# Kernel tuning notes

Measured on AMD Instinct MI355X. Metric: run time of the kernel, lower is better.

Reference implementation:

```python
import jax, jax.numpy as jnp
import numpy as np

B, CIN, N, E = 8192, 16, 96, 768
NF, EMB, NCLS = 64, 128, 210


def _p(key, shape, scale=0.05):
    return jax.random.normal(key, shape, dtype=jnp.float32) * scale


def setup_inputs() -> dict:
    key = jax.random.key(0)
    ks = jax.random.split(key, 20)
    return {
        "src": jax.random.normal(ks[0], (B, CIN, N), dtype=jnp.float32),
        "edge_index": jax.random.randint(ks[1], (2, E), 0, N, dtype=jnp.int32),
        "gcn1_w": _p(ks[2], (CIN, 64)), "gcn1_b": _p(ks[3], (64,)),
        "gcn2_w": _p(ks[4], (64, 32)), "gcn2_b": _p(ks[5], (32,)),
        "conv1_w": _p(ks[6], (NF, 32, 7)), "conv1_b": _p(ks[7], (NF,)),
        "conv2_w": _p(ks[8], (NF * 2, NF, 5)), "conv2_b": _p(ks[9], (NF * 2,)),
        "conv3_w": _p(ks[10], (NF * 4, NF * 2, 3)), "conv3_b": _p(ks[11], (NF * 4,)),
        "fc1_w": _p(ks[12], (3072, EMB)), "fc1_b": _p(ks[13], (EMB,)),
        "cls1_w": _p(ks[14], (EMB, EMB)), "cls1_b": _p(ks[15], (EMB,)),
        "cls2_w": _p(ks[16], (EMB, NCLS)), "cls2_b": _p(ks[17], (NCLS,)),
    }


def gcn_conv(x, edge_index, W, b):
    n = x.shape[1]
    loops = jnp.arange(n, dtype=edge_index.dtype)
    row = jnp.concatenate([edge_index[0], loops])  # targets
    col = jnp.concatenate([edge_index[1], loops])  # sources
    deg = jnp.zeros((n,), x.dtype).at[row].add(1.0)
    dinv = jax.lax.rsqrt(jnp.maximum(deg, 1e-12))
    norm = dinv[row] * dinv[col]                 # [E+N]
    h = x @ W                                    # [B, N, Fout]
    msgs = h[:, col, :] * norm[None, :, None]    # gather along node dim
    out = jnp.zeros_like(h).at[:, row, :].add(msgs)  # scatter-add
    return out + b


def conv1d(x, w, b, stride, pad):
    # x: [B, C, L], w: [O, C, K]
    y = jax.lax.conv_general_dilated(x, w, (stride,), [(pad, pad)],
                                     dimension_numbers=("NCH", "OIH", "NCH"))
    return y + b[None, :, None]


def reference(src, edge_index, gcn1_w, gcn1_b, gcn2_w, gcn2_b,
              conv1_w, conv1_b, conv2_w, conv2_b, conv3_w, conv3_b,
              fc1_w, fc1_b, cls1_w, cls1_b, cls2_w, cls2_b):
    x = jnp.transpose(src, (0, 2, 1))            # [B, N, CIN]
    x = jax.nn.relu(gcn_conv(x, edge_index, gcn1_w, gcn1_b))
    x = jax.nn.relu(gcn_conv(x, edge_index, gcn2_w, gcn2_b))
    x = jnp.transpose(x, (0, 2, 1))              # [B, 32, N]
    x = jax.nn.relu(conv1d(x, conv1_w, conv1_b, 2, 3))
    x = jax.nn.relu(conv1d(x, conv2_w, conv2_b, 2, 2))
    x = jax.nn.relu(conv1d(x, conv3_w, conv3_b, 2, 1))
    x = x.reshape(x.shape[0], -1)                # [B, 3072]
    feat = x @ fc1_w + fc1_b
    x = jax.nn.relu(feat)
    x = jax.nn.relu(x @ cls1_w + cls1_b)
    x = x @ cls2_w + cls2_b
    return (x, feat)
```

## Files before the change

kernel.cpp:

```cpp
#include <hip/hip_runtime.h>


typedef __attribute__((ext_vector_type(8))) short short8v;
typedef __attribute__((ext_vector_type(4))) float floatx4;

#define N_NODE 96
#define E_TOT  864
#define BATCH  8192ull

#define R0_OFF   0ull
#define R1_OFF   25165824ull
#define FR_OFF   50331648ull
#define R2_OFF   51380224ull
#define WT_OFF   52428800ull
#define W1N_OFF  (WT_OFF + 0)
#define W2N_OFF  (WT_OFF + 2048)
#define WC1_OFF  (WT_OFF + 4096)
#define WC2_OFF  (WT_OFF + 18432)
#define WC3_OFF  (WT_OFF + 59392)
#define WF1_OFF  (WT_OFF + 157696)
#define WL1_OFF  (WT_OFF + 550912)
#define WL2_OFF  (WT_OFF + 567296)
#define AH_OFF   (WT_OFF + 600064)

__device__ __forceinline__ unsigned short f2b(float f) {
    unsigned int u = __builtin_bit_cast(unsigned int, f);
    u += 0x7fffu + ((u >> 16) & 1u);
    return (unsigned short)(u >> 16);
}
__device__ __forceinline__ float b2f(unsigned short h) {
    unsigned int u = ((unsigned int)h) << 16;
    return __builtin_bit_cast(float, u);
}

__global__ void prep_all(const int* __restrict__ eidx,
                         const float* __restrict__ g1w, const float* __restrict__ g2w,
                         const float* __restrict__ w1, const float* __restrict__ w2,
                         const float* __restrict__ w3, const float* __restrict__ f1,
                         const float* __restrict__ l1, const float* __restrict__ l2,
                         unsigned short* __restrict__ wt,
                         unsigned short* __restrict__ ahf) {
    const int tid = threadIdx.x;
    if (blockIdx.x < 36) {
        __shared__ int   rowv[E_TOT];
        __shared__ int   colv[E_TOT];
        __shared__ int   rcv[E_TOT];
        __shared__ float val[E_TOT];
        __shared__ float dinv[N_NODE];
        for (int e = tid; e < E_TOT; e += 256) {
            int r, c;
            if (e < 768) { r = eidx[e]; c = eidx[768 + e]; }
            else         { r = e - 768; c = r; }
            rowv[e] = r; colv[e] = c; rcv[e] = r * 96 + c;
        }
        __syncthreads();
        if (tid < N_NODE) {
            int d = 0;
            for (int e = 0; e < E_TOT; e++) d += (rowv[e] == tid) ? 1 : 0;
            dinv[tid] = rsqrtf(fmaxf((float)d, 1e-12f));
        }
        __syncthreads();
        for (int e = tid; e < E_TOT; e += 256)
            val[e] = dinv[rowv[e]] * dinv[colv[e]];
        __syncthreads();
        int i = blockIdx.x * 256 + tid;
        int f = i >> 9, rm = i & 511;
        int ln = rm >> 3, j = rm & 7;
        int fm = f / 3, kk = f % 3;
        int row = fm * 16 + (ln & 15);
        int col = kk * 32 + (ln >> 4) * 8 + j;
        int cell = row * 96 + col;
        float a = 0.f;
        for (int e = 0; e < E_TOT; e++)
            a += (rcv[e] == cell) ? val[e] : 0.f;
        unsigned short hi = f2b(a);
        ahf[i] = hi;
        ahf[9216 + i] = f2b(a - b2f(hi));
        return;
    }
    long idx = (long)(blockIdx.x - 36) * 256 + tid;
    if (idx >= 600064) return;
    float v;
    if (idx < 2048) {
        int o = idx >> 5, c = idx & 31;
        v = (c < 16) ? g1w[c * 64 + o] : 0.f;
    } else if (idx < 4096) {
        long j = idx - 2048; int g = j >> 6, c = j & 63;
        v = g2w[c * 32 + g];
    } else {
        long base, KS;
        int region;
        if      (idx < 18432)  { base = 4096;   KS = 7;  region = 0; }
        else if (idx < 59392)  { base = 18432;  KS = 10; region = 1; }
        else if (idx < 157696) { base = 59392;  KS = 12; region = 2; }
        else if (idx < 550912) { base = 157696; KS = 96; region = 3; }
        else if (idx < 567296) { base = 550912; KS = 4;  region = 4; }
        else                   { base = 567296; KS = 4;  region = 5; }
        long local = idx - base;
        long g  = local / (KS * 512);
        long rm = local % (KS * 512);
        long ks = rm / 512;
        int lane = (int)((rm % 512) / 8);
        int j    = (int)(rm % 8);
        int quad = lane >> 4, n16 = lane & 15;
        int n = (int)(g * 16 + n16);
        int k = (int)(ks * 32 + quad * 8 + j);
        switch (region) {
            case 0: { int t = k / 32,  c = k % 32;  v = w1[n * 224 + c * 7 + t]; } break;
            case 1: { int t = k / 64,  c = k % 64;  v = w2[n * 320 + c * 5 + t]; } break;
            case 2: { int t = k / 128, c = k % 128; v = w3[n * 384 + c * 3 + t]; } break;
            case 3: { int t = k / 256, o = k % 256; v = f1[(o * 12 + t) * 128 + n]; } break;
            case 4: v = l1[k * 128 + n]; break;
            default: v = (n < 210) ? l2[k * 210 + n] : 0.f; break;
        }
    }
    wt[idx] = f2b(v);
}

__launch_bounds__(256, 4)
__global__ void gcn_fused(const float* __restrict__ src,
                          const unsigned short* __restrict__ ahf,
                          const unsigned short* __restrict__ w1n,
                          const unsigned short* __restrict__ w2n,
                          const float* __restrict__ b1,
                          const float* __restrict__ b2,
                          unsigned short* __restrict__ h2) {
    __shared__ __align__(16) unsigned short pool[4 * 4864];
    const int tid = threadIdx.x;
    const int w = tid >> 6, lane = tid & 63, quad = lane >> 4, m16 = lane & 15;
    unsigned short* P   = pool + w * 4864;
    unsigned short* XAc = P;
    unsigned short* H1W = P + 384;
    unsigned short* HWT = P + 1536;
    unsigned short* Cw  = P;
    const size_t bb = (size_t)blockIdx.x * 4 + w;

    *(unsigned int*)&XAc[(lane >> 2) * 24 + 16 + (lane & 3) * 2] = 0;

    short8v w1f[4], w2f[2][2];
    float bv1[4], bv2[2];
#pragma unroll
    for (int fn = 0; fn < 4; fn++) {
        w1f[fn] = *(const short8v*)&w1n[(fn * 16 + m16) * 32 + quad * 8];
        bv1[fn] = b1[fn * 16 + m16];
    }
#pragma unroll
    for (int fn = 0; fn < 2; fn++) {
#pragma unroll
        for (int kk = 0; kk < 2; kk++)
            w2f[fn][kk] = *(const short8v*)&w2n[(fn * 16 + m16) * 64 + kk * 32 + quad * 8];
        bv2[fn] = b2[fn * 16 + m16];
    }

    floatx4 acc[6] = {};
    const float* sB = src + bb * 1536 + (size_t)m16 * 96;
#pragma unroll
    for (int kk = 0; kk < 3; kk++) {
        float4 f0 = *(const float4*)&sB[kk * 32 + quad * 8];
        float4 f1 = *(const float4*)&sB[kk * 32 + quad * 8 + 4];
        float fv[8] = {f0.x, f0.y, f0.z, f0.w, f1.x, f1.y, f1.z, f1.w};
        short8v bh, bl;
#pragma unroll
        for (int j = 0; j < 8; j++) {
            unsigned short hi = f2b(fv[j]);
            bh[j] = (short)hi;
            bl[j] = (short)f2b(fv[j] - b2f(hi));
        }
#pragma unroll
        for (int fm = 0; fm < 6; fm++) {
            short8v ah = *(const short8v*)&ahf[((fm * 3 + kk) << 9) + lane * 8];
            short8v al = *(const short8v*)&ahf[9216 + ((fm * 3 + kk) << 9) + lane * 8];
            acc[fm] = __builtin_amdgcn_mfma_f32_16x16x32_bf16(ah, bh, acc[fm], 0, 0, 0);
            acc[fm] = __builtin_amdgcn_mfma_f32_16x16x32_bf16(al, bh, acc[fm], 0, 0, 0);
            acc[fm] = __builtin_amdgcn_mfma_f32_16x16x32_bf16(ah, bl, acc[fm], 0, 0, 0);
        }
    }

#pragma unroll
    for (int cc = 0; cc < 6; cc++) {
#pragma unroll
        for (int r = 0; r < 4; r++)
            XAc[(quad * 4 + r) * 24 + m16] = f2b(acc[cc][r]);
        short8v afr1 = *(const short8v*)&XAc[m16 * 24 + quad * 8];
        floatx4 a1[4];
#pragma unroll
        for (int fn = 0; fn < 4; fn++) {
            floatx4 zc = {0.f, 0.f, 0.f, 0.f};
            a1[fn] = __builtin_amdgcn_mfma_f32_16x16x32_bf16(afr1, w1f[fn], zc, 0, 0, 0);
        }
#pragma unroll
        for (int fn = 0; fn < 4; fn++)
#pragma unroll
            for (int r = 0; r < 4; r++)
                H1W[(quad * 4 + r) * 72 + fn * 16 + m16] =
                    f2b(fmaxf(a1[fn][r] + bv1[fn], 0.f));
        floatx4 a2[2] = {};
#pragma unroll
        for (int kk = 0; kk < 2; kk++) {
            short8v afr2 = *(const short8v*)&H1W[m16 * 72 + kk * 32 + quad * 8];
#pragma unroll
            for (int fn = 0; fn < 2; fn++)
                a2[fn] = __builtin_amdgcn_mfma_f32_16x16x32_bf16(afr2, w2f[fn][kk], a2[fn], 0, 0, 0);
        }
#pragma unroll
        for (int fn = 0; fn < 2; fn++)
#pragma unroll
            for (int r = 0; r < 4; r++)
                HWT[(fn * 16 + m16) * 104 + cc * 16 + quad * 4 + r] = f2b(a2[fn][r]);
    }

    floatx4 c2a[6][2] = {};
#pragma unroll
    for (int kk = 0; kk < 3; kk++) {
        short8v bfr[2];
#pragma unroll
        for (int fn = 0; fn < 2; fn++)
            bfr[fn] = *(const short8v*)&HWT[(fn * 16 + m16) * 104 + kk * 32 + quad * 8];
#pragma unroll
        for (int fm = 0; fm < 6; fm++) {
            short8v ah = *(const short8v*)&ahf[((fm * 3 + kk) << 9) + lane * 8];
            short8v al = *(const short8v*)&ahf[9216 + ((fm * 3 + kk) << 9) + lane * 8];
#pragma unroll
            for (int fn = 0; fn < 2; fn++) {
                c2a[fm][fn] = __builtin_amdgcn_mfma_f32_16x16x32_bf16(ah, bfr[fn], c2a[fm][fn], 0, 0, 0);
                c2a[fm][fn] = __builtin_amdgcn_mfma_f32_16x16x32_bf16(al, bfr[fn], c2a[fm][fn], 0, 0, 0);
            }
        }
    }
#pragma unroll
    for (int fm = 0; fm < 6; fm++)
#pragma unroll
        for (int fn = 0; fn < 2; fn++)
#pragma unroll
            for (int r = 0; r < 4; r++)
                Cw[(fm * 16 + quad * 4 + r) * 32 + fn * 16 + m16] =
                    f2b(fmaxf(c2a[fm][fn][r] + bv2[fn], 0.f));
#pragma unroll
    for (int it = 0; it < 6; it++) {
        int idx = it * 64 + lane;
        int node = idx >> 2, q8 = idx & 3;
        *(uint4*)&h2[((size_t)node * BATCH + bb) * 32 + q8 * 8] =
            *(const uint4*)&Cw[idx * 8];
    }
}

template<int WM, int FN, int NTAP, int CIN, int NOUT, int STRIDE, int PAD, int LIN, int BK, int MODE>
__launch_bounds__(256)
__global__ void gemm_slab(const unsigned short* __restrict__ in,
                          const unsigned short* __restrict__ wn,
                          const float* __restrict__ bias,
                          unsigned short* __restrict__ outb,
                          float* __restrict__ outf) {
    constexpr int BM  = WM * 32;
    constexpr int BN  = FN * 32;
    constexpr int BKP = BK + 8;
    constexpr int CPT = CIN / BK;
    constexpr int NC  = NTAP * CPT;
    constexpr int KS  = NTAP * CIN / 32;
    constexpr int NV  = BM * BK / 8 / 256;
    constexpr int RPV = 256 / (BK / 8);
    constexpr int SZ1 = 2 * BM * BKP;
    constexpr int SZ2 = (MODE == 4) ? 16 : BM * (BN + 8);
    constexpr int POOL = SZ1 > SZ2 ? SZ1 : SZ2;
    __shared__ __align__(16) unsigned short pool[POOL];
    const int tid = threadIdx.x;
    const size_t b0 = blockIdx.x * BM;
    const int n0 = blockIdx.y * BN;
    const int l  = blockIdx.z;
    const int w = tid >> 6, lane = tid & 63, quad = lane >> 4, m16 = lane & 15;
    const int wm = w >> 1, wq = w & 1;
    const int mbase = wm * (WM * 16), nbase = wq * (FN * 16);
    const int gw = (n0 + nbase) >> 4;
    const int lr = tid / (BK / 8);
    const int lc = tid % (BK / 8);
    floatx4 acc[WM][FN] = {};
    const short8v zz8 = {0, 0, 0, 0, 0, 0, 0, 0};

    short8v pre[NV], nxt[NV];
    {
        int pos = STRIDE * l - PAD;
        if (pos >= 0 && pos < LIN) {
            const unsigned short* ag = in + ((size_t)pos * BATCH + b0) * CIN;
#pragma unroll
            for (int v = 0; v < NV; v++)
                pre[v] = *(const short8v*)&ag[(size_t)(lr + v * RPV) * CIN + lc * 8];
        } else {
#pragma unroll
            for (int v = 0; v < NV; v++) pre[v] = zz8;
        }
#pragma unroll
        for (int v = 0; v < NV; v++)
            *(short8v*)&pool[(lr + v * RPV) * BKP + lc * 8] = pre[v];
    }
    int p = 0;
#pragma unroll
    for (int ch = 0; ch < NC; ++ch) {
        __syncthreads();
        if (ch + 1 < NC) {
            int t = (ch + 1) / CPT, inner = (ch + 1) % CPT;
            int pos = STRIDE * l + t - PAD;
            if (pos >= 0 && pos < LIN) {
                const unsigned short* ag = in + ((size_t)pos * BATCH + b0) * CIN + inner * BK;
#pragma unroll
                for (int v = 0; v < NV; v++)
                    nxt[v] = *(const short8v*)&ag[(size_t)(lr + v * RPV) * CIN + lc * 8];
            } else {
#pragma unroll
                for (int v = 0; v < NV; v++) nxt[v] = zz8;
            }
        }
        const unsigned short* As = pool + p * BM * BKP;
        const int kbase = (ch / CPT) * CIN + (ch % CPT) * BK;
#pragma unroll
        for (int kk = 0; kk < BK; kk += 32) {
            const int ksG = (kbase + kk) >> 5;
            short8v bfr[FN];
#pragma unroll
            for (int fn = 0; fn < FN; fn++)
                bfr[fn] = *(const short8v*)&wn[(((size_t)(gw + fn) * KS + ksG) << 9) + lane * 8];
#pragma unroll
            for (int fm = 0; fm < WM; fm++) {
                short8v afr = *(const short8v*)&As[(mbase + fm * 16 + m16) * BKP + kk + quad * 8];
#pragma unroll
                for (int fn = 0; fn < FN; fn++)
                    acc[fm][fn] = __builtin_amdgcn_mfma_f32_16x16x32_bf16(afr, bfr[fn], acc[fm][fn], 0, 0, 0);
            }
        }
        if (ch + 1 < NC) {
            unsigned short* Ad = pool + (p ^ 1) * BM * BKP;
#pragma unroll
            for (int v = 0; v < NV; v++)
                *(short8v*)&Ad[(lr + v * RPV) * BKP + lc * 8] = nxt[v];
        }
        p ^= 1;
    }

    if constexpr (MODE == 4) {
#pragma unroll
        for (int fn = 0; fn < FN; fn++) {
            int cg = n0 + nbase + fn * 16 + m16;
            float bv = (cg < 210) ? bias[cg] : 0.f;
            if (cg < 210) {
#pragma unroll
                for (int fm = 0; fm < WM; fm++)
#pragma unroll
                    for (int r = 0; r < 4; r++) {
                        size_t row = b0 + mbase + fm * 16 + quad * 4 + r;
                        outf[row * 210 + cg] = acc[fm][fn][r] + bv;
                    }
            }
        }
    } else {
        float bv[FN];
#pragma unroll
        for (int fn = 0; fn < FN; fn++) bv[fn] = bias[n0 + nbase + fn * 16 + m16];
        __syncthreads();
        unsigned short* Cs = pool;
#pragma unroll
        for (int fm = 0; fm < WM; fm++)
#pragma unroll
            for (int r = 0; r < 4; r++) {
                int row = mbase + fm * 16 + quad * 4 + r;
#pragma unroll
                for (int fn = 0; fn < FN; fn++)
                    Cs[row * (BN + 8) + nbase + fn * 16 + m16] =
                        f2b(fmaxf(acc[fm][fn][r] + bv[fn], 0.f));
            }
        __syncthreads();
        for (int u = tid; u < BM * (BN / 8); u += 256) {
            int r = u / (BN / 8), cc = u % (BN / 8);
            *(short8v*)&outb[((size_t)l * BATCH + b0 + r) * NOUT + n0 + cc * 8] =
                *(short8v*)&Cs[r * (BN + 8) + cc * 8];
        }
    }
}

__launch_bounds__(256)
__global__ void fc1_splitk(const unsigned short* __restrict__ c3,
                           const unsigned short* __restrict__ wf1,
                           float* __restrict__ part) {
    __shared__ __align__(16) unsigned short pool[2 * 128 * 72];
    const int tid = threadIdx.x;
    const size_t b0 = blockIdx.x * 128;
    const int kg = blockIdx.z;
    const int w = tid >> 6, lane = tid & 63, quad = lane >> 4, m16 = lane & 15;
    const int wm = w >> 1, wq = w & 1;
    const int mbase = wm * 64, nbase = wq * 64;
    const int gw = nbase >> 4;
    const int lr = tid >> 3, lc = tid & 7;
    floatx4 acc[4][4] = {};
    short8v pre[4], nxt[4];

    {
        const unsigned short* ag = c3 + ((size_t)(kg * 2) * BATCH + b0) * 256;
#pragma unroll
        for (int v = 0; v < 4; v++)
            pre[v] = *(const short8v*)&ag[(size_t)(lr + v * 32) * 256 + lc * 8];
#pragma unroll
        for (int v = 0; v < 4; v++)
            *(short8v*)&pool[(lr + v * 32) * 72 + lc * 8] = pre[v];
    }
    int p = 0;
#pragma unroll
    for (int s = 0; s < 8; ++s) {
        __syncthreads();
        if (s + 1 < 8) {
            int t = kg * 2 + ((s + 1) >> 2), inner = (s + 1) & 3;
            const unsigned short* ag = c3 + ((size_t)t * BATCH + b0) * 256 + inner * 64;
#pragma unroll
            for (int v = 0; v < 4; v++)
                nxt[v] = *(const short8v*)&ag[(size_t)(lr + v * 32) * 256 + lc * 8];
        }
        const unsigned short* As = pool + p * 128 * 72;
        const int kbase = (kg * 2 + (s >> 2)) * 256 + (s & 3) * 64;
#pragma unroll
        for (int kk = 0; kk < 64; kk += 32) {
            const int ksG = (kbase + kk) >> 5;
            short8v bfr[4];
#pragma unroll
            for (int fn = 0; fn < 4; fn++)
                bfr[fn] = *(const short8v*)&wf1[(((size_t)(gw + fn) * 96 + ksG) << 9) + lane * 8];
#pragma unroll
            for (int fm = 0; fm < 4; fm++) {
                short8v afr = *(const short8v*)&As[(mbase + fm * 16 + m16) * 72 + kk + quad * 8];
#pragma unroll
                for (int fn = 0; fn < 4; fn++)
                    acc[fm][fn] = __builtin_amdgcn_mfma_f32_16x16x32_bf16(afr, bfr[fn], acc[fm][fn], 0, 0, 0);
            }
        }
        if (s + 1 < 8) {
            unsigned short* Ad = pool + (p ^ 1) * 128 * 72;
#pragma unroll
            for (int v = 0; v < 4; v++)
                *(short8v*)&Ad[(lr + v * 32) * 72 + lc * 8] = nxt[v];
        }
        p ^= 1;
    }
    float* pg = part + (size_t)kg * BATCH * 128;
#pragma unroll
    for (int fm = 0; fm < 4; fm++)
#pragma unroll
        for (int r = 0; r < 4; r++) {
            size_t row = b0 + mbase + fm * 16 + quad * 4 + r;
#pragma unroll
            for (int fn = 0; fn < 4; fn++)
                pg[row * 128 + nbase + fn * 16 + m16] = acc[fm][fn][r];
        }
}

__launch_bounds__(256)
__global__ void fc1_reduce(const float* __restrict__ part, const float* __restrict__ bias,
                           float* __restrict__ feat, unsigned short* __restrict__ fr) {
    const size_t idx = (size_t)blockIdx.x * 256 + threadIdx.x;
    const size_t row = idx >> 5;
    const int    c4  = (int)(idx & 31);
    float4 s = *(const float4*)&bias[c4 * 4];
#pragma unroll
    for (int z = 0; z < 6; z++) {
        float4 p = *(const float4*)&part[(z * BATCH + row) * 128 + c4 * 4];
        s.x += p.x; s.y += p.y; s.z += p.z; s.w += p.w;
    }
    *(float4*)&feat[row * 128 + c4 * 4] = s;
    unsigned int d0 = (unsigned int)f2b(fmaxf(s.x, 0.f)) |
                      ((unsigned int)f2b(fmaxf(s.y, 0.f)) << 16);
    unsigned int d1 = (unsigned int)f2b(fmaxf(s.z, 0.f)) |
                      ((unsigned int)f2b(fmaxf(s.w, 0.f)) << 16);
    *(uint2*)&fr[row * 128 + c4 * 4] = make_uint2(d0, d1);
}

extern "C" void kernel_launch(void* const* d_in, const int* in_sizes, int n_in,
                              void* d_out, int out_size, void* d_ws, size_t ws_size,
                              hipStream_t stream) {
    const float* src  = (const float*)d_in[0];
    const int*   eidx = (const int*)  d_in[1];
    const float* g1w  = (const float*)d_in[2];
    const float* g1b  = (const float*)d_in[3];
    const float* g2w  = (const float*)d_in[4];
    const float* g2b  = (const float*)d_in[5];
    const float* cv1w = (const float*)d_in[6];
    const float* cv1b = (const float*)d_in[7];
    const float* cv2w = (const float*)d_in[8];
    const float* cv2b = (const float*)d_in[9];
    const float* cv3w = (const float*)d_in[10];
    const float* cv3b = (const float*)d_in[11];
    const float* fc1w = (const float*)d_in[12];
    const float* fc1b = (const float*)d_in[13];
    const float* cl1w = (const float*)d_in[14];
    const float* cl1b = (const float*)d_in[15];
    const float* cl2w = (const float*)d_in[16];
    const float* cl2b = (const float*)d_in[17];

    unsigned short* ws16 = (unsigned short*)d_ws;
    float* wsF = (float*)d_ws;
    float* out = (float*)d_out;

    unsigned short* h2  = ws16 + R0_OFF;
    unsigned short* c1  = ws16 + R1_OFF;
    unsigned short* c2  = ws16 + R0_OFF;
    unsigned short* c3  = ws16 + R1_OFF;
    float*          part = wsF;
    unsigned short* fr  = ws16 + FR_OFF;
    unsigned short* r2  = ws16 + R2_OFF;
    unsigned short* w1n = ws16 + W1N_OFF;
    unsigned short* w2n = ws16 + W2N_OFF;
    unsigned short* wc1 = ws16 + WC1_OFF;
    unsigned short* wc2 = ws16 + WC2_OFF;
    unsigned short* wc3 = ws16 + WC3_OFF;
    unsigned short* wf1 = ws16 + WF1_OFF;
    unsigned short* wl1 = ws16 + WL1_OFF;
    unsigned short* wl2 = ws16 + WL2_OFF;
    unsigned short* ahf = ws16 + AH_OFF;

    float* feat_out = out + 8192ull * 210ull;

    prep_all<<<2380, 256, 0, stream>>>(eidx, g1w, g2w, cv1w, cv2w, cv3w, fc1w, cl1w, cl2w,
                                       ws16 + WT_OFF, ahf);
    gcn_fused<<<2048, 256, 0, stream>>>(src, ahf, w1n, w2n, g1b, g2b, h2);
    gemm_slab<8, 2, 7, 32, 64, 2, 3, 96, 32, 0>
        <<<dim3(32, 1, 48), 256, 0, stream>>>(h2, wc1, cv1b, c1, nullptr);
    gemm_slab<4, 4, 5, 64, 128, 2, 2, 48, 64, 0>
        <<<dim3(64, 1, 24), 256, 0, stream>>>(c1, wc2, cv2b, c2, nullptr);
    gemm_slab<4, 4, 3, 128, 256, 2, 1, 24, 64, 0>
        <<<dim3(64, 2, 12), 256, 0, stream>>>(c2, wc3, cv3b, c3, nullptr);
    fc1_splitk<<<dim3(64, 1, 6), 256, 0, stream>>>(c3, wf1, part);
    fc1_reduce<<<1024, 256, 0, stream>>>(part, fc1b, feat_out, fr);
    gemm_slab<2, 2, 1, 128, 128, 1, 0, 1, 64, 0>
        <<<dim3(128, 2, 1), 256, 0, stream>>>(fr, wl1, cl1b, r2, nullptr);
    gemm_slab<2, 2, 1, 128, 256, 1, 0, 1, 64, 4>
        <<<dim3(128, 4, 1), 256, 0, stream>>>(r2, wl2, cl2b, nullptr, out);
}
```

Measured before the change: 334.8 us.

## Fuse fc1 reduce with classifier GEMMs and process two samples per GCN wave

Replaces the fc1 split-K reduce kernel and the two small classifier GEMM launches with one cls_fused kernel. It sums the partials, writes feat, and runs both classifier layers from shared memory, so the fr and r2 intermediates no longer go through global memory and two launches are removed. Separately, gcn_fused now handles two batch samples per wavefront, which reuses the adjacency fragment loads across both samples and halves the grid. The cost is doubled LDS per block and more registers (launch bounds lowered to 2 blocks), which lowers occupancy.

```diff
diff --git a/kernel.cpp b/kernel.cpp
--- a/kernel.cpp
+++ b/kernel.cpp
@@ -117,7 +117,7 @@
     wt[idx] = f2b(v);
 }
 
-__launch_bounds__(256, 4)
+__launch_bounds__(256, 2)
 __global__ void gcn_fused(const float* __restrict__ src,
                           const unsigned short* __restrict__ ahf,
                           const unsigned short* __restrict__ w1n,
@@ -125,17 +125,15 @@
                           const float* __restrict__ b1,
                           const float* __restrict__ b2,
                           unsigned short* __restrict__ h2) {
-    __shared__ __align__(16) unsigned short pool[4 * 4864];
+    __shared__ __align__(16) unsigned short pool[4 * 9728];
     const int tid = threadIdx.x;
     const int w = tid >> 6, lane = tid & 63, quad = lane >> 4, m16 = lane & 15;
-    unsigned short* P   = pool + w * 4864;
-    unsigned short* XAc = P;
-    unsigned short* H1W = P + 384;
-    unsigned short* HWT = P + 1536;
-    unsigned short* Cw  = P;
-    const size_t bb = (size_t)blockIdx.x * 4 + w;
-
-    *(unsigned int*)&XAc[(lane >> 2) * 24 + 16 + (lane & 3) * 2] = 0;
+    unsigned short* P = pool + w * 9728;
+    const size_t bb0 = (size_t)blockIdx.x * 8 + w * 2;
+
+#pragma unroll
+    for (int b = 0; b < 2; b++)
+        *(unsigned int*)&P[b * 4864 + (lane >> 2) * 24 + 16 + (lane & 3) * 2] = 0;
 
     short8v w1f[4], w2f[2][2];
     float bv1[4], bv2[2];
@@ -152,95 +150,133 @@
         bv2[fn] = b2[fn * 16 + m16];
     }
 
-    floatx4 acc[6] = {};
-    const float* sB = src + bb * 1536 + (size_t)m16 * 96;
+    floatx4 acc[2][6] = {};
 #pragma unroll
     for (int kk = 0; kk < 3; kk++) {
-        float4 f0 = *(const float4*)&sB[kk * 32 + quad * 8];
-        float4 f1 = *(const float4*)&sB[kk * 32 + quad * 8 + 4];
-        float fv[8] = {f0.x, f0.y, f0.z, f0.w, f1.x, f1.y, f1.z, f1.w};
-        short8v bh, bl;
-#pragma unroll
-        for (int j = 0; j < 8; j++) {
-            unsigned short hi = f2b(fv[j]);
-            bh[j] = (short)hi;
-            bl[j] = (short)f2b(fv[j] - b2f(hi));
+        short8v bh[2], bl[2];
+#pragma unroll
+        for (int b = 0; b < 2; b++) {
+            const float* sB = src + (bb0 + b) * 1536 + (size_t)m16 * 96;
+            float4 f0 = *(const float4*)&sB[kk * 32 + quad * 8];
+            float4 f1 = *(const float4*)&sB[kk * 32 + quad * 8 + 4];
+            float fv[8] = {f0.x, f0.y, f0.z, f0.w, f1.x, f1.y, f1.z, f1.w};
+#pragma unroll
+            for (int j = 0; j < 8; j++) {
+                unsigned short hi = f2b(fv[j]);
+                bh[b][j] = (short)hi;
+                bl[b][j] = (short)f2b(fv[j] - b2f(hi));
+            }
         }
 #pragma unroll
         for (int fm = 0; fm < 6; fm++) {
             short8v ah = *(const short8v*)&ahf[((fm * 3 + kk) << 9) + lane * 8];
             short8v al = *(const short8v*)&ahf[9216 + ((fm * 3 + kk) << 9) + lane * 8];
-            acc[fm] = __builtin_amdgcn_mfma_f32_16x16x32_bf16(ah, bh, acc[fm], 0, 0, 0);
-            acc[fm] = __builtin_amdgcn_mfma_f32_16x16x32_bf16(al, bh, acc[fm], 0, 0, 0);
-            acc[fm] = __builtin_amdgcn_mfma_f32_16x16x32_bf16(ah, bl, acc[fm], 0, 0, 0);
+#pragma unroll
+            for (int b = 0; b < 2; b++) {
+                acc[b][fm] = __builtin_amdgcn_mfma_f32_16x16x32_bf16(ah, bh[b], acc[b][fm], 0, 0, 0);
+                acc[b][fm] = __builtin_amdgcn_mfma_f32_16x16x32_bf16(al, bh[b], acc[b][fm], 0, 0, 0);
+                acc[b][fm] = __builtin_amdgcn_mfma_f32_16x16x32_bf16(ah, bl[b], acc[b][fm], 0, 0, 0);
+            }
         }
     }
 
 #pragma unroll
     for (int cc = 0; cc < 6; cc++) {
-#pragma unroll
-        for (int r = 0; r < 4; r++)
-            XAc[(quad * 4 + r) * 24 + m16] = f2b(acc[cc][r]);
-        short8v afr1 = *(const short8v*)&XAc[m16 * 24 + quad * 8];
-        floatx4 a1[4];
-#pragma unroll
-        for (int fn = 0; fn < 4; fn++) {
-            floatx4 zc = {0.f, 0.f, 0.f, 0.f};
-            a1[fn] = __builtin_amdgcn_mfma_f32_16x16x32_bf16(afr1, w1f[fn], zc, 0, 0, 0);
-        }
-#pragma unroll
-        for (int fn = 0; fn < 4; fn++)
+        short8v afr1[2];
+#pragma unroll
+        for (int b = 0; b < 2; b++) {
+            unsigned short* XAc = P + b * 4864;
 #pragma unroll
             for (int r = 0; r < 4; r++)
-                H1W[(quad * 4 + r) * 72 + fn * 16 + m16] =
-                    f2b(fmaxf(a1[fn][r] + bv1[fn], 0.f));
-        floatx4 a2[2] = {};
-#pragma unroll
-        for (int kk = 0; kk < 2; kk++) {
-            short8v afr2 = *(const short8v*)&H1W[m16 * 72 + kk * 32 + quad * 8];
+                XAc[(quad * 4 + r) * 24 + m16] = f2b(acc[b][cc][r]);
+            afr1[b] = *(const short8v*)&XAc[m16 * 24 + quad * 8];
+        }
+        floatx4 a1[2][4];
+#pragma unroll
+        for (int b = 0; b < 2; b++)
+#pragma unroll
+            for (int fn = 0; fn < 4; fn++) {
+                floatx4 zc = {0.f, 0.f, 0.f, 0.f};
+                a1[b][fn] = __builtin_amdgcn_mfma_f32_16x16x32_bf16(afr1[b], w1f[fn], zc, 0, 0, 0);
+            }
+#pragma unroll
+        for (int b = 0; b < 2; b++) {
+            unsigned short* H1W = P + b * 4864 + 384;
+#pragma unroll
+            for (int fn = 0; fn < 4; fn++)
+#pragma unroll
+                for (int r = 0; r < 4; r++)
+                    H1W[(quad * 4 + r) * 72 + fn * 16 + m16] =
+                        f2b(fmaxf(a1[b][fn][r] + bv1[fn], 0.f));
+        }
+        floatx4 a2[2][2] = {};
+#pragma unroll
+        for (int kk = 0; kk < 2; kk++)
+#pragma unroll
+            for (int b = 0; b < 2; b++) {
+                const unsigned short* H1W = P + b * 4864 + 384;
+                short8v afr2 = *(const short8v*)&H1W[m16 * 72 + kk * 32 + quad * 8];
+#pragma unroll
+                for (int fn = 0; fn < 2; fn++)
+                    a2[b][fn] = __builtin_amdgcn_mfma_f32_16x16x32_bf16(afr2, w2f[fn][kk], a2[b][fn], 0, 0, 0);
+            }
+#pragma unroll
+        for (int b = 0; b < 2; b++) {
+            unsigned short* HWT = P + b * 4864 + 1536;
 #pragma unroll
             for (int fn = 0; fn < 2; fn++)
-                a2[fn] = __builtin_amdgcn_mfma_f32_16x16x32_bf16(afr2, w2f[fn][kk], a2[fn], 0, 0, 0);
-        }
-#pragma unroll
-        for (int fn = 0; fn < 2; fn++)
-#pragma unroll
-            for (int r = 0; r < 4; r++)
-                HWT[(fn * 16 + m16) * 104 + cc * 16 + quad * 4 + r] = f2b(a2[fn][r]);
-    }
-
-    floatx4 c2a[6][2] = {};
+#pragma unroll
+                for (int r = 0; r < 4; r++)
+                    HWT[(fn * 16 + m16) * 104 + cc * 16 + quad * 4 + r] = f2b(a2[b][fn][r]);
+        }
+    }
+
+    floatx4 c2a[2][6][2] = {};
 #pragma unroll
     for (int kk = 0; kk < 3; kk++) {
-        short8v bfr[2];
-#pragma unroll
-        for (int fn = 0; fn < 2; fn++)
-            bfr[fn] = *(const short8v*)&HWT[(fn * 16 + m16) * 104 + kk * 32 + quad * 8];
+        short8v bfr[2][2];
+#pragma unroll
+        for (int b = 0; b < 2; b++) {
+            const unsigned short* HWT = P + b * 4864 + 1536;
+#pragma unroll
+            for (int fn = 0; fn < 2; fn++)
+                bfr[b][fn] = *(const short8v*)&HWT[(fn * 16 + m16) * 104 + kk * 32 + quad * 8];
+        }
 #pragma unroll
         for (int fm = 0; fm < 6; fm++) {
             short8v ah = *(const short8v*)&ahf[((fm * 3 + kk) << 9) + lane * 8];
             short8v al = *(const short8v*)&ahf[9216 + ((fm * 3 + kk) << 9) + lane * 8];
 #pragma unroll
-            for (int fn = 0; fn < 2; fn++) {
-                c2a[fm][fn] = __builtin_amdgcn_mfma_f32_16x16x32_bf16(ah, bfr[fn], c2a[fm][fn], 0, 0, 0);
-                c2a[fm][fn] = __builtin_amdgcn_mfma_f32_16x16x32_bf16(al, bfr[fn], c2a[fm][fn], 0, 0, 0);
-            }
-        }
-    }
-#pragma unroll
-    for (int fm = 0; fm < 6; fm++)
-#pragma unroll
-        for (int fn = 0; fn < 2; fn++)
-#pragma unroll
-            for (int r = 0; r < 4; r++)
-                Cw[(fm * 16 + quad * 4 + r) * 32 + fn * 16 + m16] =
-                    f2b(fmaxf(c2a[fm][fn][r] + bv2[fn], 0.f));
-#pragma unroll
-    for (int it = 0; it < 6; it++) {
-        int idx = it * 64 + lane;
-        int node = idx >> 2, q8 = idx & 3;
-        *(uint4*)&h2[((size_t)node * BATCH + bb) * 32 + q8 * 8] =
-            *(const uint4*)&Cw[idx * 8];
+            for (int b = 0; b < 2; b++)
+#pragma unroll
+                for (int fn = 0; fn < 2; fn++) {
+                    c2a[b][fm][fn] = __builtin_amdgcn_mfma_f32_16x16x32_bf16(ah, bfr[b][fn], c2a[b][fm][fn], 0, 0, 0);
+                    c2a[b][fm][fn] = __builtin_amdgcn_mfma_f32_16x16x32_bf16(al, bfr[b][fn], c2a[b][fm][fn], 0, 0, 0);
+                }
+        }
+    }
+#pragma unroll
+    for (int b = 0; b < 2; b++) {
+        unsigned short* Cw = P + b * 4864;
+#pragma unroll
+        for (int fm = 0; fm < 6; fm++)
+#pragma unroll
+            for (int fn = 0; fn < 2; fn++)
+#pragma unroll
+                for (int r = 0; r < 4; r++)
+                    Cw[(fm * 16 + quad * 4 + r) * 32 + fn * 16 + m16] =
+                        f2b(fmaxf(c2a[b][fm][fn][r] + bv2[fn], 0.f));
+    }
+#pragma unroll
+    for (int b = 0; b < 2; b++) {
+        const unsigned short* Cw = P + b * 4864;
+#pragma unroll
+        for (int it = 0; it < 6; it++) {
+            int idx = it * 64 + lane;
+            int node = idx >> 2, q8 = idx & 3;
+            *(uint4*)&h2[((size_t)node * BATCH + bb0 + b) * 32 + q8 * 8] =
+                *(const uint4*)&Cw[idx * 8];
+        }
     }
 }
 
@@ -449,23 +485,95 @@
 }
 
 __launch_bounds__(256)
-__global__ void fc1_reduce(const float* __restrict__ part, const float* __restrict__ bias,
-                           float* __restrict__ feat, unsigned short* __restrict__ fr) {
-    const size_t idx = (size_t)blockIdx.x * 256 + threadIdx.x;
-    const size_t row = idx >> 5;
-    const int    c4  = (int)(idx & 31);
-    float4 s = *(const float4*)&bias[c4 * 4];
-#pragma unroll
-    for (int z = 0; z < 6; z++) {
-        float4 p = *(const float4*)&part[(z * BATCH + row) * 128 + c4 * 4];
-        s.x += p.x; s.y += p.y; s.z += p.z; s.w += p.w;
-    }
-    *(float4*)&feat[row * 128 + c4 * 4] = s;
-    unsigned int d0 = (unsigned int)f2b(fmaxf(s.x, 0.f)) |
-                      ((unsigned int)f2b(fmaxf(s.y, 0.f)) << 16);
-    unsigned int d1 = (unsigned int)f2b(fmaxf(s.z, 0.f)) |
-                      ((unsigned int)f2b(fmaxf(s.w, 0.f)) << 16);
-    *(uint2*)&fr[row * 128 + c4 * 4] = make_uint2(d0, d1);
+__global__ void cls_fused(const float* __restrict__ part, const float* __restrict__ fbias,
+                          const unsigned short* __restrict__ wl1, const float* __restrict__ bl1,
+                          const unsigned short* __restrict__ wl2, const float* __restrict__ bl2,
+                          float* __restrict__ feat, float* __restrict__ outp) {
+    __shared__ __align__(16) unsigned short frL[32 * 136];
+    __shared__ __align__(16) unsigned short r2L[32 * 136];
+    const int tid = threadIdx.x;
+    const size_t b0 = (size_t)blockIdx.x * 32;
+    const int w = tid >> 6, lane = tid & 63, quad = lane >> 4, m16 = lane & 15;
+
+#pragma unroll
+    for (int u = tid; u < 1024; u += 256) {
+        int row = u >> 5, c4 = u & 31;
+        float4 s = *(const float4*)&fbias[c4 * 4];
+#pragma unroll
+        for (int z = 0; z < 6; z++) {
+            float4 p = *(const float4*)&part[((size_t)z * BATCH + b0 + row) * 128 + c4 * 4];
+            s.x += p.x; s.y += p.y; s.z += p.z; s.w += p.w;
+        }
+        *(float4*)&feat[(b0 + row) * 128 + c4 * 4] = s;
+        unsigned int d0 = (unsigned int)f2b(fmaxf(s.x, 0.f)) |
+                          ((unsigned int)f2b(fmaxf(s.y, 0.f)) << 16);
+        unsigned int d1 = (unsigned int)f2b(fmaxf(s.z, 0.f)) |
+                          ((unsigned int)f2b(fmaxf(s.w, 0.f)) << 16);
+        *(unsigned int*)&frL[row * 136 + c4 * 4]     = d0;
+        *(unsigned int*)&frL[row * 136 + c4 * 4 + 2] = d1;
+    }
+    __syncthreads();
+
+    {
+        const int nbase = w * 32;
+        floatx4 acc[2][2] = {};
+#pragma unroll
+        for (int ks = 0; ks < 4; ks++) {
+            short8v bfr[2];
+#pragma unroll
+            for (int fn = 0; fn < 2; fn++)
+                bfr[fn] = *(const short8v*)&wl1[(((size_t)(w * 2 + fn) * 4 + ks) << 9) + lane * 8];
+#pragma unroll
+            for (int fm = 0; fm < 2; fm++) {
+                short8v afr = *(const short8v*)&frL[(fm * 16 + m16) * 136 + ks * 32 + quad * 8];
+#pragma unroll
+                for (int fn = 0; fn < 2; fn++)
+                    acc[fm][fn] = __builtin_amdgcn_mfma_f32_16x16x32_bf16(afr, bfr[fn], acc[fm][fn], 0, 0, 0);
+            }
+        }
+#pragma unroll
+        for (int fm = 0; fm < 2; fm++)
+#pragma unroll
+            for (int fn = 0; fn < 2; fn++) {
+                float bv = bl1[nbase + fn * 16 + m16];
+#pragma unroll
+                for (int r = 0; r < 4; r++)
+                    r2L[(fm * 16 + quad * 4 + r) * 136 + nbase + fn * 16 + m16] =
+                        f2b(fmaxf(acc[fm][fn][r] + bv, 0.f));
+            }
+    }
+    __syncthreads();
+
+    {
+        const int nbase = w * 64;
+        floatx4 acc[2][4] = {};
+#pragma unroll
+        for (int ks = 0; ks < 4; ks++) {
+            short8v bfr[4];
+#pragma unroll
+            for (int fn = 0; fn < 4; fn++)
+                bfr[fn] = *(const short8v*)&wl2[(((size_t)(w * 4 + fn) * 4 + ks) << 9) + lane * 8];
+#pragma unroll
+            for (int fm = 0; fm < 2; fm++) {
+                short8v afr = *(const short8v*)&r2L[(fm * 16 + m16) * 136 + ks * 32 + quad * 8];
+#pragma unroll
+                for (int fn = 0; fn < 4; fn++)
+                    acc[fm][fn] = __builtin_amdgcn_mfma_f32_16x16x32_bf16(afr, bfr[fn], acc[fm][fn], 0, 0, 0);
+            }
+        }
+#pragma unroll
+        for (int fn = 0; fn < 4; fn++) {
+            int cg = nbase + fn * 16 + m16;
+            if (cg < 210) {
+                float bv = bl2[cg];
+#pragma unroll
+                for (int fm = 0; fm < 2; fm++)
+#pragma unroll
+                    for (int r = 0; r < 4; r++)
+                        outp[(b0 + fm * 16 + quad * 4 + r) * 210 + cg] = acc[fm][fn][r] + bv;
+            }
+        }
+    }
 }
 
 extern "C" void kernel_launch(void* const* d_in, const int* in_sizes, int n_in,
@@ -499,8 +607,6 @@
     unsigned short* c2  = ws16 + R0_OFF;
     unsigned short* c3  = ws16 + R1_OFF;
     float*          part = wsF;
-    unsigned short* fr  = ws16 + FR_OFF;
-    unsigned short* r2  = ws16 + R2_OFF;
     unsigned short* w1n = ws16 + W1N_OFF;
     unsigned short* w2n = ws16 + W2N_OFF;
     unsigned short* wc1 = ws16 + WC1_OFF;
@@ -515,7 +621,7 @@
 
     prep_all<<<2380, 256, 0, stream>>>(eidx, g1w, g2w, cv1w, cv2w, cv3w, fc1w, cl1w, cl2w,
                                        ws16 + WT_OFF, ahf);
-    gcn_fused<<<2048, 256, 0, stream>>>(src, ahf, w1n, w2n, g1b, g2b, h2);
+    gcn_fused<<<1024, 256, 0, stream>>>(src, ahf, w1n, w2n, g1b, g2b, h2);
     gemm_slab<8, 2, 7, 32, 64, 2, 3, 96, 32, 0>
         <<<dim3(32, 1, 48), 256, 0, stream>>>(h2, wc1, cv1b, c1, nullptr);
     gemm_slab<4, 4, 5, 64, 128, 2, 2, 48, 64, 0>
@@ -523,9 +629,5 @@
     gemm_slab<4, 4, 3, 128, 256, 2, 1, 24, 64, 0>
         <<<dim3(64, 2, 12), 256, 0, stream>>>(c2, wc3, cv3b, c3, nullptr);
     fc1_splitk<<<dim3(64, 1, 6), 256, 0, stream>>>(c3, wf1, part);
-    fc1_reduce<<<1024, 256, 0, stream>>>(part, fc1b, feat_out, fr);
-    gemm_slab<2, 2, 1, 128, 128, 1, 0, 1, 64, 0>
-        <<<dim3(128, 2, 1), 256, 0, stream>>>(fr, wl1, cl1b, r2, nullptr);
-    gemm_slab<2, 2, 1, 128, 256, 1, 0, 1, 64, 4>
-        <<<dim3(128, 4, 1), 256, 0, stream>>>(r2, wl2, cl2b, nullptr, out);
-}
+    cls_fused<<<256, 256, 0, stream>>>(part, fc1b, wl1, cl1b, wl2, cl2b, feat_out, out);
+}
```

New measurement: 329.7 us. No clear change (-1.5%).

## Fuse fc1 reduce with classifier GEMMs and shrink fc1 split-K to four

Applied to the files above, without the earlier changes.

Replaces the fc1 partial reduction and both classifier GEMM launches with one kernel. It reduces the split-K partials, writes feat, and runs cls1 and cls2 through shared memory. The fc1 split-K factor drops from 6 to 4, so each block does 12 K-steps and fewer partials are written and read. The GCN kernel now packs HWT stores into ushort4 and writes h2 directly from registers instead of staging it through LDS. That removes two launches and the intermediate round trips, at the cost of less fc1 parallelism and scattered 2-byte global stores for h2.

```diff
diff --git a/kernel.cpp b/kernel.cpp
--- a/kernel.cpp
+++ b/kernel.cpp
@@ -132,7 +132,6 @@
     unsigned short* XAc = P;
     unsigned short* H1W = P + 384;
     unsigned short* HWT = P + 1536;
-    unsigned short* Cw  = P;
     const size_t bb = (size_t)blockIdx.x * 4 + w;
 
     *(unsigned int*)&XAc[(lane >> 2) * 24 + 16 + (lane & 3) * 2] = 0;
@@ -203,10 +202,12 @@
                 a2[fn] = __builtin_amdgcn_mfma_f32_16x16x32_bf16(afr2, w2f[fn][kk], a2[fn], 0, 0, 0);
         }
 #pragma unroll
-        for (int fn = 0; fn < 2; fn++)
-#pragma unroll
-            for (int r = 0; r < 4; r++)
-                HWT[(fn * 16 + m16) * 104 + cc * 16 + quad * 4 + r] = f2b(a2[fn][r]);
+        for (int fn = 0; fn < 2; fn++) {
+            ushort4 pk;
+            pk.x = f2b(a2[fn][0]); pk.y = f2b(a2[fn][1]);
+            pk.z = f2b(a2[fn][2]); pk.w = f2b(a2[fn][3]);
+            *(ushort4*)&HWT[(fn * 16 + m16) * 104 + cc * 16 + quad * 4] = pk;
+        }
     }
 
     floatx4 c2a[6][2] = {};
@@ -232,16 +233,11 @@
 #pragma unroll
         for (int fn = 0; fn < 2; fn++)
 #pragma unroll
-            for (int r = 0; r < 4; r++)
-                Cw[(fm * 16 + quad * 4 + r) * 32 + fn * 16 + m16] =
+            for (int r = 0; r < 4; r++) {
+                int node = fm * 16 + quad * 4 + r;
+                h2[((size_t)node * BATCH + bb) * 32 + fn * 16 + m16] =
                     f2b(fmaxf(c2a[fm][fn][r] + bv2[fn], 0.f));
-#pragma unroll
-    for (int it = 0; it < 6; it++) {
-        int idx = it * 64 + lane;
-        int node = idx >> 2, q8 = idx & 3;
-        *(uint4*)&h2[((size_t)node * BATCH + bb) * 32 + q8 * 8] =
-            *(const uint4*)&Cw[idx * 8];
-    }
+            }
 }
 
 template<int WM, int FN, int NTAP, int CIN, int NOUT, int STRIDE, int PAD, int LIN, int BK, int MODE>
@@ -392,7 +388,7 @@
     short8v pre[4], nxt[4];
 
     {
-        const unsigned short* ag = c3 + ((size_t)(kg * 2) * BATCH + b0) * 256;
+        const unsigned short* ag = c3 + ((size_t)(kg * 3) * BATCH + b0) * 256;
 #pragma unroll
         for (int v = 0; v < 4; v++)
             pre[v] = *(const short8v*)&ag[(size_t)(lr + v * 32) * 256 + lc * 8];
@@ -402,17 +398,17 @@
     }
     int p = 0;
 #pragma unroll
-    for (int s = 0; s < 8; ++s) {
-        __syncthreads();
-        if (s + 1 < 8) {
-            int t = kg * 2 + ((s + 1) >> 2), inner = (s + 1) & 3;
+    for (int s = 0; s < 12; ++s) {
+        __syncthreads();
+        if (s + 1 < 12) {
+            int t = kg * 3 + ((s + 1) >> 2), inner = (s + 1) & 3;
             const unsigned short* ag = c3 + ((size_t)t * BATCH + b0) * 256 + inner * 64;
 #pragma unroll
             for (int v = 0; v < 4; v++)
                 nxt[v] = *(const short8v*)&ag[(size_t)(lr + v * 32) * 256 + lc * 8];
         }
         const unsigned short* As = pool + p * 128 * 72;
-        const int kbase = (kg * 2 + (s >> 2)) * 256 + (s & 3) * 64;
+        const int kbase = (kg * 3 + (s >> 2)) * 256 + (s & 3) * 64;
 #pragma unroll
         for (int kk = 0; kk < 64; kk += 32) {
             const int ksG = (kbase + kk) >> 5;
@@ -428,7 +424,7 @@
                     acc[fm][fn] = __builtin_amdgcn_mfma_f32_16x16x32_bf16(afr, bfr[fn], acc[fm][fn], 0, 0, 0);
             }
         }
-        if (s + 1 < 8) {
+        if (s + 1 < 12) {
             unsigned short* Ad = pool + (p ^ 1) * 128 * 72;
 #pragma unroll
             for (int v = 0; v < 4; v++)
@@ -449,23 +445,95 @@
 }
 
 __launch_bounds__(256)
-__global__ void fc1_reduce(const float* __restrict__ part, const float* __restrict__ bias,
-                           float* __restrict__ feat, unsigned short* __restrict__ fr) {
-    const size_t idx = (size_t)blockIdx.x * 256 + threadIdx.x;
-    const size_t row = idx >> 5;
-    const int    c4  = (int)(idx & 31);
-    float4 s = *(const float4*)&bias[c4 * 4];
-#pragma unroll
-    for (int z = 0; z < 6; z++) {
-        float4 p = *(const float4*)&part[(z * BATCH + row) * 128 + c4 * 4];
-        s.x += p.x; s.y += p.y; s.z += p.z; s.w += p.w;
-    }
-    *(float4*)&feat[row * 128 + c4 * 4] = s;
-    unsigned int d0 = (unsigned int)f2b(fmaxf(s.x, 0.f)) |
-                      ((unsigned int)f2b(fmaxf(s.y, 0.f)) << 16);
-    unsigned int d1 = (unsigned int)f2b(fmaxf(s.z, 0.f)) |
-                      ((unsigned int)f2b(fmaxf(s.w, 0.f)) << 16);
-    *(uint2*)&fr[row * 128 + c4 * 4] = make_uint2(d0, d1);
+__global__ void cls_fused(const float* __restrict__ part, const float* __restrict__ fbias,
+                          const unsigned short* __restrict__ wl1, const float* __restrict__ bl1,
+                          const unsigned short* __restrict__ wl2, const float* __restrict__ bl2,
+                          float* __restrict__ feat, float* __restrict__ outp) {
+    __shared__ __align__(16) unsigned short frL[32 * 136];
+    __shared__ __align__(16) unsigned short r2L[32 * 136];
+    const int tid = threadIdx.x;
+    const size_t b0 = (size_t)blockIdx.x * 32;
+    const int w = tid >> 6, lane = tid & 63, quad = lane >> 4, m16 = lane & 15;
+
+#pragma unroll
+    for (int u = tid; u < 1024; u += 256) {
+        int row = u >> 5, c4 = u & 31;
+        float4 s = *(const float4*)&fbias[c4 * 4];
+#pragma unroll
+        for (int z = 0; z < 4; z++) {
+            float4 p = *(const float4*)&part[((size_t)z * BATCH + b0 + row) * 128 + c4 * 4];
+            s.x += p.x; s.y += p.y; s.z += p.z; s.w += p.w;
+        }
+        *(float4*)&feat[(b0 + row) * 128 + c4 * 4] = s;
+        unsigned int d0 = (unsigned int)f2b(fmaxf(s.x, 0.f)) |
+                          ((unsigned int)f2b(fmaxf(s.y, 0.f)) << 16);
+        unsigned int d1 = (unsigned int)f2b(fmaxf(s.z, 0.f)) |
+                          ((unsigned int)f2b(fmaxf(s.w, 0.f)) << 16);
+        *(unsigned int*)&frL[row * 136 + c4 * 4]     = d0;
+        *(unsigned int*)&frL[row * 136 + c4 * 4 + 2] = d1;
+    }
+    __syncthreads();
+
+    {
+        const int nbase = w * 32;
+        floatx4 acc[2][2] = {};
+#pragma unroll
+        for (int ks = 0; ks < 4; ks++) {
+            short8v bfr[2];
+#pragma unroll
+            for (int fn = 0; fn < 2; fn++)
+                bfr[fn] = *(const short8v*)&wl1[(((size_t)(w * 2 + fn) * 4 + ks) << 9) + lane * 8];
+#pragma unroll
+            for (int fm = 0; fm < 2; fm++) {
+                short8v afr = *(const short8v*)&frL[(fm * 16 + m16) * 136 + ks * 32 + quad * 8];
+#pragma unroll
+                for (int fn = 0; fn < 2; fn++)
+                    acc[fm][fn] = __builtin_amdgcn_mfma_f32_16x16x32_bf16(afr, bfr[fn], acc[fm][fn], 0, 0, 0);
+            }
+        }
+#pragma unroll
+        for (int fm = 0; fm < 2; fm++)
+#pragma unroll
+            for (int fn = 0; fn < 2; fn++) {
+                float bv = bl1[nbase + fn * 16 + m16];
+#pragma unroll
+                for (int r = 0; r < 4; r++)
+                    r2L[(fm * 16 + quad * 4 + r) * 136 + nbase + fn * 16 + m16] =
+                        f2b(fmaxf(acc[fm][fn][r] + bv, 0.f));
+            }
+    }
+    __syncthreads();
+
+    {
+        const int nbase = w * 64;
+        floatx4 acc[2][4] = {};
+#pragma unroll
+        for (int ks = 0; ks < 4; ks++) {
+            short8v bfr[4];
+#pragma unroll
+            for (int fn = 0; fn < 4; fn++)
+                bfr[fn] = *(const short8v*)&wl2[(((size_t)(w * 4 + fn) * 4 + ks) << 9) + lane * 8];
+#pragma unroll
+            for (int fm = 0; fm < 2; fm++) {
+                short8v afr = *(const short8v*)&r2L[(fm * 16 + m16) * 136 + ks * 32 + quad * 8];
+#pragma unroll
+                for (int fn = 0; fn < 4; fn++)
+                    acc[fm][fn] = __builtin_amdgcn_mfma_f32_16x16x32_bf16(afr, bfr[fn], acc[fm][fn], 0, 0, 0);
+            }
+        }
+#pragma unroll
+        for (int fn = 0; fn < 4; fn++) {
+            int cg = nbase + fn * 16 + m16;
+            if (cg < 210) {
+                float bv = bl2[cg];
+#pragma unroll
+                for (int fm = 0; fm < 2; fm++)
+#pragma unroll
+                    for (int r = 0; r < 4; r++)
+                        outp[(b0 + fm * 16 + quad * 4 + r) * 210 + cg] = acc[fm][fn][r] + bv;
+            }
+        }
+    }
 }
 
 extern "C" void kernel_launch(void* const* d_in, const int* in_sizes, int n_in,
@@ -499,8 +567,6 @@
     unsigned short* c2  = ws16 + R0_OFF;
     unsigned short* c3  = ws16 + R1_OFF;
     float*          part = wsF;
-    unsigned short* fr  = ws16 + FR_OFF;
-    unsigned short* r2  = ws16 + R2_OFF;
     unsigned short* w1n = ws16 + W1N_OFF;
     unsigned short* w2n = ws16 + W2N_OFF;
     unsigned short* wc1 = ws16 + WC1_OFF;
@@ -522,10 +588,6 @@
         <<<dim3(64, 1, 24), 256, 0, stream>>>(c1, wc2, cv2b, c2, nullptr);
     gemm_slab<4, 4, 3, 128, 256, 2, 1, 24, 64, 0>
         <<<dim3(64, 2, 12), 256, 0, stream>>>(c2, wc3, cv3b, c3, nullptr);
-    fc1_splitk<<<dim3(64, 1, 6), 256, 0, stream>>>(c3, wf1, part);
-    fc1_reduce<<<1024, 256, 0, stream>>>(part, fc1b, feat_out, fr);
-    gemm_slab<2, 2, 1, 128, 128, 1, 0, 1, 64, 0>
-        <<<dim3(128, 2, 1), 256, 0, stream>>>(fr, wl1, cl1b, r2, nullptr);
-    gemm_slab<2, 2, 1, 128, 256, 1, 0, 1, 64, 4>
-        <<<dim3(128, 4, 1), 256, 0, stream>>>(r2, wl2, cl2b, nullptr, out);
-}
+    fc1_splitk<<<dim3(64, 1, 4), 256, 0, stream>>>(c3, wf1, part);
+    cls_fused<<<256, 256, 0, stream>>>(part, fc1b, wl1, cl1b, wl2, cl2b, feat_out, out);
+}
```

After: 329.9 us. No clear change (-1.5%).
